# Kernel tuning notes

Measured on AMD Instinct MI355X. Metric: run time of the kernel, lower is better.

The kernel has to match this reference:

```python
import jax, jax.numpy as jnp
import numpy as np

N_NODES = 100000
D_FEAT = 128
N_EDGES = 625000
EDGE_EMBED = 32
EPS = 1e-8  # torch F.cosine_similarity default eps


def setup_inputs() -> dict:
    key = jax.random.key(0)
    ks = jax.random.split(key, 7)
    x = jax.random.normal(ks[0], (N_NODES, D_FEAT), dtype=jnp.float32)
    edge_index = jax.random.randint(ks[1], (2, N_EDGES), 0, N_NODES, dtype=jnp.int64)
    edge_attr = jax.random.normal(ks[2], (N_EDGES, 4), dtype=jnp.float32)
    # encoder params: Linear(5,18) -> ReLU -> Linear(18, EDGE_EMBED) -> ReLU
    W1 = jax.random.normal(ks[3], (5, 18), dtype=jnp.float32) * (1.0 / np.sqrt(5))
    b1 = jax.random.normal(ks[4], (18,), dtype=jnp.float32) * 0.01
    W2 = jax.random.normal(ks[5], (18, EDGE_EMBED), dtype=jnp.float32) * (1.0 / np.sqrt(18))
    b2 = jax.random.normal(ks[6], (EDGE_EMBED,), dtype=jnp.float32) * 0.01
    return {"x": x, "edge_index": edge_index, "edge_attr": edge_attr,
            "W1": W1, "b1": b1, "W2": W2, "b2": b2}


def reference(x, edge_index, edge_attr, W1, b1, W2, b2):
    src = edge_index[0]
    tgt = edge_index[1]
    s = x[src]  # [E, d] gather
    t = x[tgt]  # [E, d] gather
    # cosine similarity along dim=1, torch semantics with eps clamp on norms
    dot = jnp.sum(s * t, axis=1)
    ns = jnp.maximum(jnp.linalg.norm(s, axis=1), EPS)
    nt = jnp.maximum(jnp.linalg.norm(t, axis=1), EPS)
    cos = (dot / (ns * nt))[:, None]  # [E, 1]
    feats = jnp.concatenate([edge_attr, cos], axis=1)  # [E, 5]
    h = jax.nn.relu(feats @ W1 + b1)
    out = jax.nn.relu(h @ W2 + b2)  # [E, EDGE_EMBED]
    return out
```

## Files before the change

kernel.cpp:

```cpp
#include <hip/hip_runtime.h>
#include <stdint.h>

#define D_FEAT 128
#define H1 18
#define H2 32
#define EPS 1e-8f

typedef float f32x4 __attribute__((ext_vector_type(4)));
typedef float f32x2 __attribute__((ext_vector_type(2)));

__global__ __launch_bounds__(256) void prep_kernel(
    const float* __restrict__ x,
    uint32_t* __restrict__ xq,
    int n_nodes)
{
    const int lane = threadIdx.x & 63;
    const int sub = lane & 31;
    const int half = lane >> 5;
    const int wavesPerBlock = blockDim.x >> 6;
    const long long wv = (long long)blockIdx.x * wavesPerBlock + (threadIdx.x >> 6);
    const int node = (int)(2 * wv + half);
    if (node >= n_nodes) return;

    const f32x4 v = __builtin_nontemporal_load(
        reinterpret_cast<const f32x4*>(x + (size_t)node * D_FEAT) + sub);
    float ss = v[0] * v[0] + v[1] * v[1] + v[2] * v[2] + v[3] * v[3];
    #pragma unroll
    for (int m = 16; m >= 1; m >>= 1) ss += __shfl_xor(ss, m);
    const float r = 1.0f / fmaxf(sqrtf(ss), EPS);

    int p = 0;
    p = __builtin_amdgcn_cvt_pk_fp8_f32(v[0] * r, v[1] * r, p, false);
    p = __builtin_amdgcn_cvt_pk_fp8_f32(v[2] * r, v[3] * r, p, true);
    xq[(size_t)node * 32 + sub] = (uint32_t)p;
}

__device__ __forceinline__ float dot16f8(uint4 s, uint4 t) {
    float d = 0.f;
    #define TERM(SW, TW)                                                   \
        {                                                                  \
            const f32x2 a0 = __builtin_amdgcn_cvt_pk_f32_fp8((int)(SW), false); \
            const f32x2 a1 = __builtin_amdgcn_cvt_pk_f32_fp8((int)(SW), true);  \
            const f32x2 c0 = __builtin_amdgcn_cvt_pk_f32_fp8((int)(TW), false); \
            const f32x2 c1 = __builtin_amdgcn_cvt_pk_f32_fp8((int)(TW), true);  \
            d = fmaf(a0[0], c0[0], d);                                     \
            d = fmaf(a0[1], c0[1], d);                                     \
            d = fmaf(a1[0], c1[0], d);                                     \
            d = fmaf(a1[1], c1[1], d);                                     \
        }
    TERM(s.x, t.x)
    TERM(s.y, t.y)
    TERM(s.z, t.z)
    TERM(s.w, t.w)
    #undef TERM
    return d;
}

__global__ __launch_bounds__(256) void edge_kernel(
    const uint4* __restrict__ xq,
    const int* __restrict__ edge_index,
    const float* __restrict__ edge_attr,
    const float* __restrict__ W1, const float* __restrict__ b1,
    const float* __restrict__ W2, const float* __restrict__ b2,
    float* __restrict__ out, int n_edges)
{
    __shared__ int sIdx[4][64];
    __shared__ int tIdx[4][64];
    __shared__ float dotb[4][64];

    const int lane = threadIdx.x & 63;
    const int w = threadIdx.x >> 6;
    const int g = lane >> 3;
    const int k = lane & 7;
    const long long nBursts = ((long long)n_edges + 63) >> 6;
    const long long burst = (long long)blockIdx.x * 4 + w;
    if (burst >= nBursts) return;

    const f32x4* __restrict__ eav = reinterpret_cast<const f32x4*>(edge_attr);
    const f32x4* __restrict__ W2v = reinterpret_cast<const f32x4*>(W2);
    const f32x4* __restrict__ b2v = reinterpret_cast<const f32x4*>(b2);

    const long long e = (burst << 6) + lane;
    const bool act = e < (long long)n_edges;
    {
        int sL = 0, tL = 0;
        if (act) {
            sL = edge_index[e];
            tL = edge_index[(long long)n_edges + e];
        }
        sIdx[w][lane] = sL;
        tIdx[w][lane] = tL;
    }

    uint4 su[8], tu[8];
    #pragma unroll
    for (int s = 0; s < 8; ++s) {
        const int eg = s * 8 + g;
        su[s] = xq[(size_t)sIdx[w][eg] * 8 + k];
        tu[s] = xq[(size_t)tIdx[w][eg] * 8 + k];
    }
    f32x4 attr = (f32x4)0.f;
    if (act) attr = eav[e];

    __builtin_amdgcn_sched_barrier(0);

    #pragma unroll
    for (int s = 0; s < 8; ++s) {
        const int eg = s * 8 + g;
        float d = dot16f8(su[s], tu[s]);
        d += __shfl_xor(d, 1);
        d += __shfl_xor(d, 2);
        d += __shfl_xor(d, 4);
        if (k == 0) dotb[w][eg] = d;
    }

    const float cosv = dotb[w][lane];

    float h[H1];
    #pragma unroll
    for (int i = 0; i < H1; ++i) {
        float v = b1[i];
        v = fmaf(attr[0], W1[0 * H1 + i], v);
        v = fmaf(attr[1], W1[1 * H1 + i], v);
        v = fmaf(attr[2], W1[2 * H1 + i], v);
        v = fmaf(attr[3], W1[3 * H1 + i], v);
        v = fmaf(cosv,    W1[4 * H1 + i], v);
        h[i] = fmaxf(v, 0.f);
    }

    if (act) {
        f32x4* op = reinterpret_cast<f32x4*>(out + (size_t)e * H2);
        #pragma unroll
        for (int jg = 0; jg < 8; ++jg) {
            f32x4 a = b2v[jg];
            #pragma unroll
            for (int i = 0; i < H1; ++i)
                a += h[i] * W2v[i * 8 + jg];
            #pragma unroll
            for (int c = 0; c < 4; ++c)
                a[c] = fmaxf(a[c], 0.f);
            op[jg] = a;
        }
    }
}

__device__ __forceinline__ float mlp_out32(
    const float4 ea, float cosv,
    const float* __restrict__ sW1, const float* __restrict__ sb1,
    const float* __restrict__ sW2, const float* __restrict__ sb2,
    int sub, int base)
{
    const float f[5] = { ea.x, ea.y, ea.z, ea.w, cosv };
    float hval = 0.f;
    if (sub < H1) {
        hval = sb1[sub];
        #pragma unroll
        for (int kk = 0; kk < 5; ++kk) hval = fmaf(f[kk], sW1[kk * H1 + sub], hval);
        hval = fmaxf(hval, 0.f);
    }
    float acc = sb2[sub];
    #pragma unroll
    for (int i = 0; i < H1; ++i)
        acc = fmaf(__shfl(hval, base + i), sW2[i * H2 + sub], acc);
    return fmaxf(acc, 0.f);
}

__global__ __launch_bounds__(256) void edge_encoder_fp32(
    const float* __restrict__ x,
    const int* __restrict__ edge_index,
    const float* __restrict__ edge_attr,
    const float* __restrict__ W1, const float* __restrict__ b1,
    const float* __restrict__ W2, const float* __restrict__ b2,
    float* __restrict__ out, int n_edges)
{
    __shared__ float sW1[5 * H1];
    __shared__ float sb1[H1];
    __shared__ float sW2[H1 * H2];
    __shared__ float sb2[H2];
    for (int i = threadIdx.x; i < 5 * H1; i += blockDim.x) sW1[i] = W1[i];
    for (int i = threadIdx.x; i < H1; i += blockDim.x) sb1[i] = b1[i];
    for (int i = threadIdx.x; i < H1 * H2; i += blockDim.x) sW2[i] = W2[i];
    for (int i = threadIdx.x; i < H2; i += blockDim.x) sb2[i] = b2[i];
    __syncthreads();

    const int lane = threadIdx.x & 63;
    const int sub = lane & 31;
    const int base = lane & 32;
    const int wavesPerBlock = blockDim.x >> 6;
    const int waveId = blockIdx.x * wavesPerBlock + (threadIdx.x >> 6);
    const int totalWaves = gridDim.x * wavesPerBlock;

    for (long long gg = waveId; 2 * gg < (long long)n_edges; gg += totalWaves) {
        const long long e = 2 * gg + (lane >> 5);
        const bool active = (e < (long long)n_edges);
        float dot = 0.f, ss = 0.f, tt = 0.f;
        float4 ea = make_float4(0.f, 0.f, 0.f, 0.f);
        if (active) {
            const int srcN = edge_index[e];
            const int tgtN = edge_index[(long long)n_edges + e];
            const float4 s4 = *reinterpret_cast<const float4*>(
                x + (size_t)srcN * D_FEAT + (size_t)sub * 4);
            const float4 t4 = *reinterpret_cast<const float4*>(
                x + (size_t)tgtN * D_FEAT + (size_t)sub * 4);
            dot = s4.x * t4.x + s4.y * t4.y + s4.z * t4.z + s4.w * t4.w;
            ss  = s4.x * s4.x + s4.y * s4.y + s4.z * s4.z + s4.w * s4.w;
            tt  = t4.x * t4.x + t4.y * t4.y + t4.z * t4.z + t4.w * t4.w;
            ea = *reinterpret_cast<const float4*>(edge_attr + e * 4);
        }
        #pragma unroll
        for (int m = 16; m >= 1; m >>= 1) {
            dot += __shfl_xor(dot, m);
            ss  += __shfl_xor(ss, m);
            tt  += __shfl_xor(tt, m);
        }
        const float cosv = dot / (fmaxf(sqrtf(ss), EPS) * fmaxf(sqrtf(tt), EPS));
        const float o = mlp_out32(ea, cosv, sW1, sb1, sW2, sb2, sub, base);
        if (active) out[e * H2 + sub] = o;
    }
}

extern "C" void kernel_launch(void* const* d_in, const int* in_sizes, int n_in,
                              void* d_out, int out_size, void* d_ws, size_t ws_size,
                              hipStream_t stream) {
    const float* x         = (const float*)d_in[0];
    const int*   edge_idx  = (const int*)d_in[1];
    const float* edge_attr = (const float*)d_in[2];
    const float* W1        = (const float*)d_in[3];
    const float* b1        = (const float*)d_in[4];
    const float* W2        = (const float*)d_in[5];
    const float* b2        = (const float*)d_in[6];
    float* out = (float*)d_out;

    const int n_nodes = in_sizes[0] / D_FEAT;
    const int n_edges = in_sizes[1] / 2;

    const size_t xq_bytes = (size_t)n_nodes * D_FEAT;

    if (ws_size >= xq_bytes) {
        uint32_t* xq = (uint32_t*)d_ws;
        const int block = 256;
        const int prep_grid = (n_nodes + 7) / 8;
        prep_kernel<<<prep_grid, block, 0, stream>>>(x, xq, n_nodes);

        const long long nBursts = ((long long)n_edges + 63) >> 6;
        const int grid = (int)((nBursts + 3) / 4);
        edge_kernel<<<grid, block, 0, stream>>>(
            (const uint4*)xq, edge_idx, edge_attr,
            W1, b1, W2, b2, out, n_edges);
    } else {
        edge_encoder_fp32<<<2048, 256, 0, stream>>>(
            x, edge_idx, edge_attr, W1, b1, W2, b2, out, n_edges);
    }
}
```

Baseline: 62.57 us.

## Gather fp8 node rows directly into LDS via global_load_lds

Replaces register-destination gathers of quantized node rows with global_load_lds transfers into a 64KB per-block LDS staging buffer, then reads the rows back from LDS for the dot products. Row indices are now broadcast with wave shuffles instead of going through shared-memory index arrays. The aim is to cut VGPR pressure and let more loads be in flight, at the cost of large LDS use that limits occupancy to few blocks per CU, plus an extra LDS read pass. An unused bf16 conversion helper is also added.

```diff
diff --git a/kernel.cpp b/kernel.cpp
--- a/kernel.cpp
+++ b/kernel.cpp
@@ -8,6 +8,11 @@
 
 typedef float f32x4 __attribute__((ext_vector_type(4)));
 typedef float f32x2 __attribute__((ext_vector_type(2)));
+
+__device__ __forceinline__ uint32_t f32_to_bf16_rne(float f) {
+    uint32_t u = __float_as_uint(f);
+    return (u + 0x7fffu + ((u >> 16) & 1u)) >> 16;
+}
 
 __global__ __launch_bounds__(256) void prep_kernel(
     const float* __restrict__ x,
@@ -57,15 +62,14 @@
 }
 
 __global__ __launch_bounds__(256) void edge_kernel(
-    const uint4* __restrict__ xq,
+    const uint8_t* __restrict__ xq,
     const int* __restrict__ edge_index,
     const float* __restrict__ edge_attr,
     const float* __restrict__ W1, const float* __restrict__ b1,
     const float* __restrict__ W2, const float* __restrict__ b2,
     float* __restrict__ out, int n_edges)
 {
-    __shared__ int sIdx[4][64];
-    __shared__ int tIdx[4][64];
+    __shared__ __align__(16) uint8_t stage[4][16384];
     __shared__ float dotb[4][64];
 
     const int lane = threadIdx.x & 63;
@@ -82,32 +86,43 @@
 
     const long long e = (burst << 6) + lane;
     const bool act = e < (long long)n_edges;
-    {
-        int sL = 0, tL = 0;
-        if (act) {
-            sL = edge_index[e];
-            tL = edge_index[(long long)n_edges + e];
-        }
-        sIdx[w][lane] = sL;
-        tIdx[w][lane] = tL;
-    }
-
-    uint4 su[8], tu[8];
+    int sL = 0, tL = 0;
+    if (act) {
+        sL = edge_index[e];
+        tL = edge_index[(long long)n_edges + e];
+    }
+
     #pragma unroll
     for (int s = 0; s < 8; ++s) {
         const int eg = s * 8 + g;
-        su[s] = xq[(size_t)sIdx[w][eg] * 8 + k];
-        tu[s] = xq[(size_t)tIdx[w][eg] * 8 + k];
-    }
+        const int sRow = __shfl(sL, eg);
+        const int tRow = __shfl(tL, eg);
+        const uint8_t* gs = xq + (size_t)sRow * 128 + (size_t)k * 16;
+        const uint8_t* gt = xq + (size_t)tRow * 128 + (size_t)k * 16;
+        __builtin_amdgcn_global_load_lds(
+            (const __attribute__((address_space(1))) void*)gs,
+            (__attribute__((address_space(3))) void*)&stage[w][s * 2048],
+            16, 0, 0);
+        __builtin_amdgcn_global_load_lds(
+            (const __attribute__((address_space(1))) void*)gt,
+            (__attribute__((address_space(3))) void*)&stage[w][s * 2048 + 1024],
+            16, 0, 0);
+    }
+
     f32x4 attr = (f32x4)0.f;
     if (act) attr = eav[e];
 
+    asm volatile("s_waitcnt vmcnt(0)" ::: "memory");
     __builtin_amdgcn_sched_barrier(0);
 
     #pragma unroll
     for (int s = 0; s < 8; ++s) {
         const int eg = s * 8 + g;
-        float d = dot16f8(su[s], tu[s]);
+        const uint4 su = *reinterpret_cast<const uint4*>(
+            &stage[w][s * 2048 + (size_t)lane * 16]);
+        const uint4 tu = *reinterpret_cast<const uint4*>(
+            &stage[w][s * 2048 + 1024 + (size_t)lane * 16]);
+        float d = dot16f8(su, tu);
         d += __shfl_xor(d, 1);
         d += __shfl_xor(d, 2);
         d += __shfl_xor(d, 4);
@@ -245,7 +260,7 @@
         const long long nBursts = ((long long)n_edges + 63) >> 6;
         const int grid = (int)((nBursts + 3) / 4);
         edge_kernel<<<grid, block, 0, stream>>>(
-            (const uint4*)xq, edge_idx, edge_attr,
+            (const uint8_t*)xq, edge_idx, edge_attr,
             W1, b1, W2, b2, out, n_edges);
     } else {
         edge_encoder_fp32<<<2048, 256, 0, stream>>>(
```

New measurement: 74.38 us. 1.19x slower.
